# Kernel optimization log

Measured on AMD Instinct MI355X. Metric: run time of the kernel, lower is better.

The kernel has to match this reference:

```python
import jax, jax.numpy as jnp
import numpy as np

B, S, D, H = 4, 2048, 768, 12
DK = D // H


def setup_inputs() -> dict:
    key = jax.random.key(0)
    ks = jax.random.split(key, 13)
    s = 1.0 / np.sqrt(D)
    inp = {
        "q": jax.random.normal(ks[0], (B, S, D), jnp.float32),
        "k": jax.random.normal(ks[1], (B, S, D), jnp.float32),
        "v": jax.random.normal(ks[2], (B, S, D), jnp.float32),
        "mask": jax.random.randint(ks[3], (B, S), 0, 2, jnp.int32),
        "Wq": jax.random.normal(ks[4], (D, D), jnp.float32) * s,
        "bq": jnp.zeros((D,), jnp.float32),
        "Wk": jax.random.normal(ks[5], (D, D), jnp.float32) * s,
        "bk": jnp.zeros((D,), jnp.float32),
        "Wv": jax.random.normal(ks[6], (D, D), jnp.float32) * s,
        "bv": jnp.zeros((D,), jnp.float32),
        "Wo": jax.random.normal(ks[7], (D, D), jnp.float32) * s,
        "bo": jnp.zeros((D,), jnp.float32),
    }
    return inp


def reference(q, k, v, mask, Wq, bq, Wk, bk, Wv, bv, Wo, bo):
    b, s, d = q.shape
    # projections (torch Linear: x @ W.T + b), split into heads: [b, h, s, dk]
    Q = (q @ Wq.T + bq).reshape(b, s, H, DK).transpose(0, 2, 1, 3)
    K = (k @ Wk.T + bk).reshape(b, s, H, DK).transpose(0, 2, 1, 3)
    V = (v @ Wv.T + bv).reshape(b, s, H, DK).transpose(0, 2, 1, 3)
    scores = jnp.einsum("bhqd,bhkd->bhqk", Q, K) / jnp.sqrt(jnp.float32(DK))
    # mask [b,s] -> [b,1,s,1]: masks whole query rows (faithful to source)
    scores = jnp.where(mask[:, None, :, None] == 0, jnp.float32(-1e9), scores)
    attn = jax.nn.softmax(scores, axis=-1)  # dropout is identity at inference
    out = jnp.einsum("bhqk,bhkd->bhqd", attn, V)
    concat = out.transpose(0, 2, 1, 3).reshape(b, s, d)
    return concat @ Wo.T + bo
```

## Files before the change

### kernel.cpp

```cpp
#include <hip/hip_runtime.h>

typedef _Float16 f16;
typedef f16 f16x4 __attribute__((ext_vector_type(4)));
typedef f16 f16x8 __attribute__((ext_vector_type(8)));
typedef float f32x4 __attribute__((ext_vector_type(4)));

#define B_ 4
#define S_ 2048
#define D_ 768
#define H_ 12
#define DK_ 64

__device__ __forceinline__ void dma16(const f16* g, f16* l) {
    __builtin_amdgcn_global_load_lds(
        (__attribute__((address_space(1))) void*)(uintptr_t)g,
        (__attribute__((address_space(3))) void*)l, 16, 0, 0);
}

struct Cvt7 { const float* s[7]; f16* d[7]; int n[7]; };

__global__ __launch_bounds__(256) void cvt7_kernel(Cvt7 a)
{
    const int z = blockIdx.y;
    int i = (blockIdx.x * 256 + threadIdx.x) * 8;
    if (i >= a.n[z]) return;
    const float* __restrict__ s = a.s[z];
    float4 x = *(const float4*)(s + i);
    float4 y = *(const float4*)(s + i + 4);
    f16x8 h = {(f16)x.x, (f16)x.y, (f16)x.z, (f16)x.w,
               (f16)y.x, (f16)y.y, (f16)y.z, (f16)y.w};
    *(f16x8*)(a.d[z] + i) = h;
}

struct GemmArgs { const f16* A; const f16* W; const float* bias; float scale; void* C; int mode; };
struct GemmArgs3 { GemmArgs g[3]; };

__global__ __launch_bounds__(256, 4) void gemm_k(GemmArgs3 args)
{
    const int z = blockIdx.z;
    const f16* __restrict__ A = args.g[z].A;
    const f16* __restrict__ W = args.g[z].W;
    const float* __restrict__ bias = args.g[z].bias;
    const float scale = args.g[z].scale;
    const int mode = args.g[z].mode;

    __shared__ __align__(16) f16 As[128 * 64];
    __shared__ __align__(16) f16 Bs[128 * 64];

    const int tid = threadIdx.x, lane = tid & 63, w = tid >> 6;
    const int l15 = lane & 15, lg = lane >> 4;
    const int wm = (w >> 1) * 64, wn = (w & 1) * 64;
    const int m0 = blockIdx.y * 128, n0 = blockIdx.x * 128;

    const int lrow8 = lane >> 3;
    const int lchk8 = (lane & 7) ^ lrow8;
    const f16* gA = A + (size_t)(m0 + w * 32 + lrow8) * D_ + lchk8 * 8;
    const f16* gB = W + (size_t)(n0 + w * 32 + lrow8) * D_ + lchk8 * 8;

    f32x4 acc[4][4] = {};

    for (int kt = 0; kt < D_; kt += 64) {
        __syncthreads();
#pragma unroll
        for (int c = 0; c < 4; ++c) {
            dma16(gA + (size_t)(c * 8) * D_ + kt, &As[(w * 4 + c) * 512]);
            dma16(gB + (size_t)(c * 8) * D_ + kt, &Bs[(w * 4 + c) * 512]);
        }
        __syncthreads();
#pragma unroll
        for (int kk = 0; kk < 2; ++kk) {
            const int chk = ((kk * 4 + lg) ^ (l15 & 7)) * 8;
            f16x8 af[4], bf[4];
#pragma unroll
            for (int i = 0; i < 4; ++i)
                af[i] = *(const f16x8*)&As[(wm + i * 16 + l15) * 64 + chk];
#pragma unroll
            for (int j = 0; j < 4; ++j)
                bf[j] = *(const f16x8*)&Bs[(wn + j * 16 + l15) * 64 + chk];
#pragma unroll
            for (int i = 0; i < 4; ++i)
#pragma unroll
                for (int j = 0; j < 4; ++j)
                    acc[i][j] = __builtin_amdgcn_mfma_f32_16x16x32_f16(
                        af[i], bf[j], acc[i][j], 0, 0, 0);
        }
    }

    if (mode == 1) {
#pragma unroll
        for (int j = 0; j < 4; ++j) {
            int col = n0 + wn + j * 16 + l15;
            float bb = bias[col];
#pragma unroll
            for (int i = 0; i < 4; ++i) {
                int row = m0 + wm + i * 16 + lg * 4;
                int bI = row >> 11, sl = row & (S_ - 1);
                f16x4 o = {(f16)(acc[i][j][0] + bb), (f16)(acc[i][j][1] + bb),
                           (f16)(acc[i][j][2] + bb), (f16)(acc[i][j][3] + bb)};
                *(f16x4*)&((f16*)args.g[z].C)[((size_t)bI * D_ + col) * S_ + sl] = o;
            }
        }
    } else if (mode == 0) {
#pragma unroll
        for (int j = 0; j < 4; ++j) {
            int col = n0 + wn + j * 16 + l15;
            float bb = bias[col];
#pragma unroll
            for (int i = 0; i < 4; ++i) {
                int row = m0 + wm + i * 16 + lg * 4;
#pragma unroll
                for (int r = 0; r < 4; ++r)
                    ((f16*)args.g[z].C)[(size_t)(row + r) * D_ + col] =
                        (f16)((acc[i][j][r] + bb) * scale);
            }
        }
    } else {
#pragma unroll
        for (int j = 0; j < 4; ++j) {
            int col = n0 + wn + j * 16 + l15;
            float bb = bias[col];
#pragma unroll
            for (int i = 0; i < 4; ++i) {
                int row = m0 + wm + i * 16 + lg * 4;
#pragma unroll
                for (int r = 0; r < 4; ++r)
                    ((float*)args.g[z].C)[(size_t)(row + r) * D_ + col] =
                        acc[i][j][r] + bb;
            }
        }
    }
}

__global__ __launch_bounds__(256, 3) void attn_k(
    const f16* __restrict__ Qh, const f16* __restrict__ Kh,
    const f16* __restrict__ VhT, const int* __restrict__ mask,
    f16* __restrict__ O)
{
    __shared__ __align__(16) f16 Ks[128 * 64];
    __shared__ __align__(16) f16 Vt[64 * 128];
    const int tid = threadIdx.x, lane = tid & 63, w = tid >> 6;
    const int l15 = lane & 15, lg = lane >> 4;

    const int bid = blockIdx.x;
    const int g8 = bid & 7, j5 = bid >> 3;
    const int head_lin = g8 * 6 + (j5 >> 4);
    const int qt = j5 & 15;
    const int b = head_lin / H_, h = head_lin % H_;
    const int q0 = qt * 128;
    const int rowbase = b * S_;
    const int col0 = h * DK_;

    const int lrow8 = lane >> 3;
    const int lchk8 = (lane & 7) ^ lrow8;

    {
        const f16* Qbase = Qh + (size_t)(rowbase + q0 + w * 32 + lrow8) * D_ + col0 + lchk8 * 8;
#pragma unroll
        for (int c = 0; c < 4; ++c)
            dma16(Qbase + (size_t)(c * 8) * D_, &Ks[(w * 4 + c) * 512]);
    }
    __syncthreads();
    f16x8 qf[2][2];
#pragma unroll
    for (int ns = 0; ns < 2; ++ns) {
        float mf = (mask[rowbase + q0 + w * 32 + ns * 16 + l15] != 0) ? 1.0f : 0.0f;
#pragma unroll
        for (int kk = 0; kk < 2; ++kk) {
            f16x8 t = *(const f16x8*)&Ks[(w * 32 + ns * 16 + l15) * 64 +
                                         (((kk * 4 + lg) ^ (l15 & 7)) * 8)];
#pragma unroll
            for (int e = 0; e < 8; ++e) t[e] = (f16)((float)t[e] * mf);
            qf[ns][kk] = t;
        }
    }

    const f16* Kbase = Kh + (size_t)rowbase * D_ + col0;
    const f16* Vbase = VhT + ((size_t)b * D_ + col0) * S_;
    const int vrow4 = lane >> 4;
    const int vchk = lane & 15;

    float lrun[2] = {0.f, 0.f};
    f32x4 acc[4][2] = {};

    for (int t = 0; t < S_ / 128; ++t) {
        const int k0 = t * 128;
        __syncthreads();
#pragma unroll
        for (int c = 0; c < 4; ++c)
            dma16(Kbase + (size_t)(k0 + w * 32 + c * 8 + lrow8) * D_ + lchk8 * 8,
                  &Ks[(w * 4 + c) * 512]);
#pragma unroll
        for (int c = 0; c < 4; ++c) {
            int o = w * 4 + c;
            int drow = o * 4 + vrow4;
            int gchk = vchk ^ (drow & 15);
            dma16(Vbase + (size_t)drow * S_ + k0 + gchk * 8, &Vt[o * 512]);
        }
        __syncthreads();

        f32x4 sf[8][2] = {};
#pragma unroll
        for (int kk = 0; kk < 2; ++kk) {
            const int chk = ((kk * 4 + lg) ^ (l15 & 7)) * 8;
#pragma unroll
            for (int ms = 0; ms < 8; ++ms) {
                f16x8 kf = *(const f16x8*)&Ks[(ms * 16 + l15) * 64 + chk];
                sf[ms][0] = __builtin_amdgcn_mfma_f32_16x16x32_f16(
                    kf, qf[0][kk], sf[ms][0], 0, 0, 0);
                sf[ms][1] = __builtin_amdgcn_mfma_f32_16x16x32_f16(
                    kf, qf[1][kk], sf[ms][1], 0, 0, 0);
            }
        }

        f16x4 pf[8][2];
#pragma unroll
        for (int ns = 0; ns < 2; ++ns) {
            float rs = 0.f;
#pragma unroll
            for (int ms = 0; ms < 8; ++ms) {
                float p0 = __builtin_exp2f(sf[ms][ns][0]);
                float p1 = __builtin_exp2f(sf[ms][ns][1]);
                float p2 = __builtin_exp2f(sf[ms][ns][2]);
                float p3 = __builtin_exp2f(sf[ms][ns][3]);
                rs += (p0 + p1) + (p2 + p3);
                pf[ms][ns] = {(f16)p0, (f16)p1, (f16)p2, (f16)p3};
            }
            rs += __shfl_xor(rs, 16, 64);
            rs += __shfl_xor(rs, 32, 64);
            lrun[ns] += rs;
        }

#pragma unroll
        for (int c = 0; c < 8; ++c) {
            const int pchk = (((c * 2 + (lg >> 1)) ^ l15) * 8) + (lg & 1) * 4;
#pragma unroll
            for (int i = 0; i < 4; ++i) {
                f16x4 vf = *(const f16x4*)&Vt[(i * 16 + l15) * 128 + pchk];
                acc[i][0] = __builtin_amdgcn_mfma_f32_16x16x16f16(
                    vf, pf[c][0], acc[i][0], 0, 0, 0);
                acc[i][1] = __builtin_amdgcn_mfma_f32_16x16x16f16(
                    vf, pf[c][1], acc[i][1], 0, 0, 0);
            }
        }
    }

#pragma unroll
    for (int ns = 0; ns < 2; ++ns) {
        float inv = 1.0f / lrun[ns];
        size_t qrow = (size_t)(rowbase + q0 + w * 32 + ns * 16 + l15);
#pragma unroll
        for (int i = 0; i < 4; ++i) {
            f32x4 o = acc[i][ns] * inv;
            f16x4 ho = {(f16)o[0], (f16)o[1], (f16)o[2], (f16)o[3]};
            *(f16x4*)&O[qrow * D_ + col0 + i * 16 + lg * 4] = ho;
        }
    }
}

extern "C" void kernel_launch(void* const* d_in, const int* in_sizes, int n_in,
                              void* d_out, int out_size, void* d_ws, size_t ws_size,
                              hipStream_t stream)
{
    const float* q    = (const float*)d_in[0];
    const float* k    = (const float*)d_in[1];
    const float* v    = (const float*)d_in[2];
    const int*   mask = (const int*)d_in[3];
    const float* Wq   = (const float*)d_in[4];
    const float* bq   = (const float*)d_in[5];
    const float* Wk   = (const float*)d_in[6];
    const float* bk   = (const float*)d_in[7];
    const float* Wv   = (const float*)d_in[8];
    const float* bv   = (const float*)d_in[9];
    const float* Wo   = (const float*)d_in[10];
    const float* bo   = (const float*)d_in[11];

    const size_t nQKV = (size_t)B_ * S_ * D_;
    const size_t nW   = (size_t)D_ * D_;

    f16* qh  = (f16*)d_ws;
    f16* kh  = qh + nQKV;
    f16* vh  = kh + nQKV;
    f16* Wqh = vh + nQKV;
    f16* Wkh = Wqh + nW;
    f16* Wvh = Wkh + nW;
    f16* Woh = Wvh + nW;
    f16* Qp  = Woh + nW;
    f16* Kp  = Qp + nQKV;
    f16* VpT = Kp + nQKV;
    f16* Cp  = VpT + nQKV;

    Cvt7 cv = {{q, k, v, Wq, Wk, Wv, Wo},
               {qh, kh, vh, Wqh, Wkh, Wvh, Woh},
               {(int)nQKV, (int)nQKV, (int)nQKV, (int)nW, (int)nW, (int)nW, (int)nW}};
    cvt7_kernel<<<dim3((int)(nQKV / 8 / 256), 7), 256, 0, stream>>>(cv);

    GemmArgs3 g1 = {{{qh, Wqh, bq, 1.44269504f / 8.0f, (void*)Qp, 0},
                     {kh, Wkh, bk, 1.0f, (void*)Kp, 0},
                     {vh, Wvh, bv, 1.0f, (void*)VpT, 1}}};
    gemm_k<<<dim3(6, 64, 3), 256, 0, stream>>>(g1);

    attn_k<<<dim3(768), 256, 0, stream>>>(Qp, Kp, VpT, mask, Cp);

    GemmArgs3 g2 = {{{Cp, Woh, bo, 1.0f, d_out, 2},
                     {Cp, Woh, bo, 1.0f, d_out, 2},
                     {Cp, Woh, bo, 1.0f, d_out, 2}}};
    gemm_k<<<dim3(6, 64, 1), 256, 0, stream>>>(g2);
}
```

Measured before the change: 293.3 us.

## Double-buffer K/V tiles and switch attention to 32x32 MFMA

Rewrites the attention inner loop to stream 64-key K/V tiles into two alternating LDS buffers, prefetching tile t+2 while tile t is computed. Manual vmcnt waits replace the two full syncthreads per iteration. It also moves both QK and PV to 32x32 MFMA instructions, packs probabilities with cvt_pkrtz, and changes the V swizzle layout. The aims are to hide global-load latency and cut LDS fragment reads per FLOP, at the cost of fragile manual waitcnt ordering and a changed rounding mode for the probabilities.

```diff
diff --git a/kernel.cpp b/kernel.cpp
--- a/kernel.cpp
+++ b/kernel.cpp
@@ -1,9 +1,12 @@
 #include <hip/hip_runtime.h>
 
 typedef _Float16 f16;
+typedef f16 f16x2 __attribute__((ext_vector_type(2)));
+typedef __fp16 h16x2 __attribute__((ext_vector_type(2)));
 typedef f16 f16x4 __attribute__((ext_vector_type(4)));
 typedef f16 f16x8 __attribute__((ext_vector_type(8)));
 typedef float f32x4 __attribute__((ext_vector_type(4)));
+typedef float f32x16 __attribute__((ext_vector_type(16)));
 
 #define B_ 4
 #define S_ 2048
@@ -136,10 +139,9 @@
     const f16* __restrict__ VhT, const int* __restrict__ mask,
     f16* __restrict__ O)
 {
-    __shared__ __align__(16) f16 Ks[128 * 64];
-    __shared__ __align__(16) f16 Vt[64 * 128];
+    __shared__ __align__(16) f16 lds[2][8192];
     const int tid = threadIdx.x, lane = tid & 63, w = tid >> 6;
-    const int l15 = lane & 15, lg = lane >> 4;
+    const int l31 = lane & 31, lhi = lane >> 5;
 
     const int bid = blockIdx.x;
     const int g8 = bid & 7, j5 = bid >> 3;
@@ -157,104 +159,108 @@
         const f16* Qbase = Qh + (size_t)(rowbase + q0 + w * 32 + lrow8) * D_ + col0 + lchk8 * 8;
 #pragma unroll
         for (int c = 0; c < 4; ++c)
-            dma16(Qbase + (size_t)(c * 8) * D_, &Ks[(w * 4 + c) * 512]);
+            dma16(Qbase + (size_t)(c * 8) * D_, &lds[0][(w * 4 + c) * 512]);
     }
     __syncthreads();
-    f16x8 qf[2][2];
-#pragma unroll
-    for (int ns = 0; ns < 2; ++ns) {
-        float mf = (mask[rowbase + q0 + w * 32 + ns * 16 + l15] != 0) ? 1.0f : 0.0f;
-#pragma unroll
-        for (int kk = 0; kk < 2; ++kk) {
-            f16x8 t = *(const f16x8*)&Ks[(w * 32 + ns * 16 + l15) * 64 +
-                                         (((kk * 4 + lg) ^ (l15 & 7)) * 8)];
-#pragma unroll
-            for (int e = 0; e < 8; ++e) t[e] = (f16)((float)t[e] * mf);
-            qf[ns][kk] = t;
-        }
-    }
+    f16x8 qf[4];
+    {
+        const int qrow = w * 32 + l31;
+        const f16 mf = (f16)((mask[rowbase + q0 + qrow] != 0) ? 1.0f : 0.0f);
+#pragma unroll
+        for (int dc = 0; dc < 4; ++dc) {
+            f16x8 t = *(const f16x8*)&lds[0][qrow * 64 +
+                                            (((dc * 2 + lhi) ^ (qrow & 7)) * 8)];
+            qf[dc] = t * mf;
+        }
+    }
+    __syncthreads();
 
     const f16* Kbase = Kh + (size_t)rowbase * D_ + col0;
     const f16* Vbase = VhT + ((size_t)b * D_ + col0) * S_;
-    const int vrow4 = lane >> 4;
-    const int vchk = lane & 15;
-
-    float lrun[2] = {0.f, 0.f};
-    f32x4 acc[4][2] = {};
-
-    for (int t = 0; t < S_ / 128; ++t) {
-        const int k0 = t * 128;
-        __syncthreads();
-#pragma unroll
-        for (int c = 0; c < 4; ++c)
-            dma16(Kbase + (size_t)(k0 + w * 32 + c * 8 + lrow8) * D_ + lchk8 * 8,
-                  &Ks[(w * 4 + c) * 512]);
-#pragma unroll
-        for (int c = 0; c < 4; ++c) {
-            int o = w * 4 + c;
-            int drow = o * 4 + vrow4;
-            int gchk = vchk ^ (drow & 15);
-            dma16(Vbase + (size_t)drow * S_ + k0 + gchk * 8, &Vt[o * 512]);
-        }
-        __syncthreads();
-
-        f32x4 sf[8][2] = {};
-#pragma unroll
-        for (int kk = 0; kk < 2; ++kk) {
-            const int chk = ((kk * 4 + lg) ^ (l15 & 7)) * 8;
-#pragma unroll
-            for (int ms = 0; ms < 8; ++ms) {
-                f16x8 kf = *(const f16x8*)&Ks[(ms * 16 + l15) * 64 + chk];
-                sf[ms][0] = __builtin_amdgcn_mfma_f32_16x16x32_f16(
-                    kf, qf[0][kk], sf[ms][0], 0, 0, 0);
-                sf[ms][1] = __builtin_amdgcn_mfma_f32_16x16x32_f16(
-                    kf, qf[1][kk], sf[ms][1], 0, 0, 0);
-            }
-        }
-
-        f16x4 pf[8][2];
-#pragma unroll
-        for (int ns = 0; ns < 2; ++ns) {
-            float rs = 0.f;
-#pragma unroll
-            for (int ms = 0; ms < 8; ++ms) {
-                float p0 = __builtin_exp2f(sf[ms][ns][0]);
-                float p1 = __builtin_exp2f(sf[ms][ns][1]);
-                float p2 = __builtin_exp2f(sf[ms][ns][2]);
-                float p3 = __builtin_exp2f(sf[ms][ns][3]);
-                rs += (p0 + p1) + (p2 + p3);
-                pf[ms][ns] = {(f16)p0, (f16)p1, (f16)p2, (f16)p3};
-            }
-            rs += __shfl_xor(rs, 16, 64);
-            rs += __shfl_xor(rs, 32, 64);
-            lrun[ns] += rs;
-        }
-
-#pragma unroll
-        for (int c = 0; c < 8; ++c) {
-            const int pchk = (((c * 2 + (lg >> 1)) ^ l15) * 8) + (lg & 1) * 4;
-#pragma unroll
-            for (int i = 0; i < 4; ++i) {
-                f16x4 vf = *(const f16x4*)&Vt[(i * 16 + l15) * 128 + pchk];
-                acc[i][0] = __builtin_amdgcn_mfma_f32_16x16x16f16(
-                    vf, pf[c][0], acc[i][0], 0, 0, 0);
-                acc[i][1] = __builtin_amdgcn_mfma_f32_16x16x16f16(
-                    vf, pf[c][1], acc[i][1], 0, 0, 0);
-            }
-        }
-    }
-
-#pragma unroll
-    for (int ns = 0; ns < 2; ++ns) {
-        float inv = 1.0f / lrun[ns];
-        size_t qrow = (size_t)(rowbase + q0 + w * 32 + ns * 16 + l15);
-#pragma unroll
-        for (int i = 0; i < 4; ++i) {
-            f32x4 o = acc[i][ns] * inv;
-            f16x4 ho = {(f16)o[0], (f16)o[1], (f16)o[2], (f16)o[3]};
-            *(f16x4*)&O[qrow * D_ + col0 + i * 16 + lg * 4] = ho;
-        }
-    }
+
+#define STAGE(j)                                                              \
+    {                                                                         \
+        f16* Ksd = &lds[(j) & 1][0];                                          \
+        f16* Vtd = &lds[(j) & 1][4096];                                       \
+        const int k0s = (j) * 64;                                             \
+        _Pragma("unroll")                                                     \
+        for (int c = 0; c < 2; ++c) {                                         \
+            int o = w * 2 + c;                                                \
+            dma16(Kbase + (size_t)(k0s + o * 8 + lrow8) * D_ + lchk8 * 8,     \
+                  &Ksd[o * 512]);                                             \
+            dma16(Vbase + (size_t)(o * 8 + lrow8) * S_ + k0s + lchk8 * 8,     \
+                  &Vtd[o * 512]);                                             \
+        }                                                                     \
+    }
+
+    STAGE(0);
+    STAGE(1);
+
+    float rsum = 0.f;
+    f32x16 acc[2] = {};
+
+#pragma unroll 2
+    for (int t = 0; t < 32; ++t) {
+        const f16* Ksc = &lds[t & 1][0];
+        const f16* Vtc = &lds[t & 1][4096];
+
+        asm volatile("s_waitcnt vmcnt(4)" ::: "memory");
+        __builtin_amdgcn_s_barrier();
+
+#pragma unroll
+        for (int kc = 0; kc < 2; ++kc) {
+            f32x16 s = {};
+#pragma unroll
+            for (int dc = 0; dc < 4; ++dc) {
+                f16x8 kf = *(const f16x8*)&Ksc[(kc * 32 + l31) * 64 +
+                                               (((dc * 2 + lhi) ^ (lane & 7)) * 8)];
+                s = __builtin_amdgcn_mfma_f32_32x32x16_f16(kf, qf[dc], s, 0, 0, 0);
+            }
+            f16x4 pb[4];
+#pragma unroll
+            for (int g = 0; g < 4; ++g) {
+                float e0 = __builtin_exp2f(s[4 * g + 0]);
+                float e1 = __builtin_exp2f(s[4 * g + 1]);
+                float e2 = __builtin_exp2f(s[4 * g + 2]);
+                float e3 = __builtin_exp2f(s[4 * g + 3]);
+                f16x2 lo = __builtin_bit_cast(f16x2, __builtin_amdgcn_cvt_pkrtz(e0, e1));
+                f16x2 hi = __builtin_bit_cast(f16x2, __builtin_amdgcn_cvt_pkrtz(e2, e3));
+                rsum += (float)lo[0] + (float)lo[1] + (float)hi[0] + (float)hi[1];
+                f16x4 p;
+                p[0] = lo[0]; p[1] = lo[1]; p[2] = hi[0]; p[3] = hi[1];
+                pb[g] = p;
+            }
+#pragma unroll
+            for (int dc2 = 0; dc2 < 2; ++dc2)
+#pragma unroll
+                for (int g = 0; g < 4; ++g) {
+                    int kb = kc * 4 + g;
+                    f16x4 vf = *(const f16x4*)&Vtc[(dc2 * 32 + l31) * 64 +
+                                                   ((kb ^ (lane & 7)) * 8) + lhi * 4];
+                    acc[dc2] = __builtin_amdgcn_mfma_f32_32x32x8f16(
+                        vf, pb[g], acc[dc2], 0, 0, 0);
+                }
+        }
+
+        asm volatile("s_waitcnt lgkmcnt(0)" ::: "memory");
+        __builtin_amdgcn_s_barrier();
+        if (t + 2 < 32) STAGE(t + 2);
+    }
+
+    rsum += __shfl_xor(rsum, 32, 64);
+    const float inv = 1.0f / rsum;
+    const size_t qrow = (size_t)(rowbase + q0 + w * 32 + l31);
+#pragma unroll
+    for (int dc2 = 0; dc2 < 2; ++dc2)
+#pragma unroll
+        for (int grp = 0; grp < 4; ++grp) {
+            f16x4 ho = {(f16)(acc[dc2][4 * grp + 0] * inv),
+                        (f16)(acc[dc2][4 * grp + 1] * inv),
+                        (f16)(acc[dc2][4 * grp + 2] * inv),
+                        (f16)(acc[dc2][4 * grp + 3] * inv)};
+            *(f16x4*)&O[qrow * D_ + col0 + dc2 * 32 + grp * 8 + lhi * 4] = ho;
+        }
+#undef STAGE
 }
 
 extern "C" void kernel_launch(void* const* d_in, const int* in_sizes, int n_in,
```

New measurement: 292.9 us. About the same (-0.1%).
